# Kernel optimization log

Measured on AMD Instinct MI355X. Metric: run time of the kernel, lower is better.

The kernel has to match this reference:

```python
import jax, jax.numpy as jnp
import numpy as np

MARGIN = 0.1
EPS = 1e-8  # torch CosineSimilarity eps


def setup_inputs() -> dict:
    key = jax.random.key(0)
    k1, k2 = jax.random.split(key)
    embeddings = jax.random.normal(k1, (8192, 128), dtype=jnp.float32)
    labels = jax.random.randint(k2, (8192,), 0, 100, dtype=jnp.int64 if jax.config.jax_enable_x64 else jnp.int32)
    return {"embeddings": embeddings, "labels": labels}


def reference(embeddings, labels):
    n = embeddings.shape[0]
    # Normalize rows (torch: x / max(||x||, eps))
    norm = jnp.linalg.norm(embeddings, axis=1, keepdims=True)
    en = embeddings / jnp.maximum(norm, EPS)
    # Full cosine-similarity matrix via one GEMM: [n, n]
    sim = jnp.einsum('id,jd->ij', en, en)
    same = labels[:, None] == labels[None, :]
    pair_loss = jnp.where(same, jax.nn.relu(1.0 - sim), jax.nn.relu(sim - MARGIN))
    # Sum over i < j (strict upper triangle), matching the double loop
    upper = jnp.triu(jnp.ones((n, n), dtype=pair_loss.dtype), k=1)
    loss = jnp.sum(pair_loss * upper) / (n * (n - 1))
    return loss
```

## Files before the change

kernel.cpp:

```cpp
#include <hip/hip_runtime.h>
#include <hip/hip_bf16.h>


typedef __attribute__((ext_vector_type(8))) short short8;
typedef __attribute__((ext_vector_type(4))) float f32x4;

#define DIM 128
#define MARGIN 0.1f
#define CHUNK 4

typedef const void __attribute__((address_space(1)))* gas_ptr;
typedef void __attribute__((address_space(3)))* las_ptr;

static __device__ __forceinline__ void load16_to_lds(const void* g, void* l) {
    __builtin_amdgcn_global_load_lds((gas_ptr)g, (las_ptr)l, 16, 0, 0);
}

static __device__ __forceinline__ unsigned short f2bf(float f) {
    unsigned int u = __builtin_bit_cast(unsigned int, f);
    u += 0x7FFFu + ((u >> 16) & 1u);
    return (unsigned short)(u >> 16);
}

static __device__ __forceinline__ void stage64(const short* __restrict__ en, int row0,
                                               short* buf, int tid) {
    const char* src = (const char*)(en + (size_t)row0 * DIM);
    char* dst = (char*)buf;
    const int r_lo = tid >> 4;
    const int s    = tid & 15;
    #pragma unroll
    for (int p = 0; p < 4; ++p) {
        const int r  = p * 16 + r_lo;
        const int sc = (s ^ (r & 7)) << 4;
        load16_to_lds(src + (size_t)r * 256 + sc, dst + r * 256 + s * 16);
    }
}

static __device__ __forceinline__ short8 read_frag(const short* buf, int row, int slot) {
    const int ps = slot ^ (row & 7);
    return *(const short8*)(buf + row * DIM + ps * 8);
}

__global__ void __launch_bounds__(256) norm_bf16_kernel(const float* __restrict__ e,
                                                        unsigned int* __restrict__ en_packed) {
    const int row  = blockIdx.x * 4 + (threadIdx.x >> 6);
    const int lane = threadIdx.x & 63;
    const float2 v = *reinterpret_cast<const float2*>(e + row * DIM + lane * 2);
    float s = v.x * v.x + v.y * v.y;
    #pragma unroll
    for (int off = 32; off; off >>= 1) s += __shfl_xor(s, off, 64);
    const float scale = 1.0f / fmaxf(sqrtf(s), 1e-8f);
    const unsigned int lo = f2bf(v.x * scale);
    const unsigned int hi = f2bf(v.y * scale);
    en_packed[row * (DIM / 2) + lane] = (hi << 16) | lo;
}

__global__ void __launch_bounds__(256, 3)
tri_loss_kernel(const short* __restrict__ en, const int* __restrict__ labels,
                float* __restrict__ partials, int nt) {
    __shared__ __align__(16) short buf[2][64 * DIM];
    __shared__ float wsum[4];

    int t  = blockIdx.x;
    int bi = 0, cnt = (nt + CHUNK - 1) / CHUNK;
    #pragma unroll 1
    while (t >= cnt) { t -= cnt; ++bi; cnt = (nt - bi + CHUNK - 1) / CHUNK; }
    const int jbase = bi + t * CHUNK;
    const int nsub  = 2 * min(CHUNK, nt - jbase);

    const int tid  = threadIdx.x;
    const int lane = tid & 63;
    const int wid  = tid >> 6;
    const int wr   = wid >> 1, wc = wid & 1;
    const int lm   = lane & 15;
    const int hi   = lane >> 4;

    stage64(en, bi * 128,      &buf[0][0], tid);
    stage64(en, bi * 128 + 64, &buf[1][0], tid);

    const int r0w = bi * 128 + wr * 64;
    int4 li[4];
    #pragma unroll
    for (int m = 0; m < 4; ++m) li[m] = *(const int4*)(labels + r0w + m * 16 + hi * 4);

    __syncthreads();

    short8 a[4][4];
    const short* Abuf = &buf[wr][0];
    #pragma unroll
    for (int m = 0; m < 4; ++m)
        #pragma unroll
        for (int ks = 0; ks < 4; ++ks)
            a[m][ks] = read_frag(Abuf, m * 16 + lm, hi + ks * 4);

    __syncthreads();

    stage64(en, jbase * 128, &buf[0][0], tid);
    __syncthreads();

    float lsum = 0.0f;
    const int rb = hi * 4;

    #pragma unroll 1
    for (int s = 0; s < nsub; ++s) {
        const short* cur = &buf[s & 1][0];
        if (s + 1 < nsub)
            stage64(en, jbase * 128 + (s + 1) * 64, &buf[(s + 1) & 1][0], tid);

        const int c0 = jbase * 128 + s * 64 + wc * 32;
        int labj[2];
        labj[0] = labels[c0 + lm];
        labj[1] = labels[c0 + 16 + lm];

        f32x4 acc[4][2] = {};
        #pragma unroll
        for (int ks = 0; ks < 4; ++ks) {
            short8 b[2];
            b[0] = read_frag(cur, wc * 32 + lm,      hi + ks * 4);
            b[1] = read_frag(cur, wc * 32 + 16 + lm, hi + ks * 4);
            #pragma unroll
            for (int m = 0; m < 4; ++m)
                #pragma unroll
                for (int n = 0; n < 2; ++n)
                    acc[m][n] = __builtin_amdgcn_mfma_f32_16x16x32_bf16(a[m][ks], b[n], acc[m][n], 0, 0, 0);
        }

        const bool diag = (jbase == bi) && (s < 2);
        #pragma unroll
        for (int m = 0; m < 4; ++m) {
            #pragma unroll
            for (int r = 0; r < 4; ++r) {
                const int i   = r0w + m * 16 + rb + r;
                const int l_i = ((const int*)&li[m])[r];
                #pragma unroll
                for (int n = 0; n < 2; ++n) {
                    const int j  = c0 + n * 16 + lm;
                    const float sv = acc[m][n][r];
                    const float t2 = (l_i == labj[n]) ? (1.0f - sv) : (sv - MARGIN);
                    const float v  = fmaxf(t2, 0.0f);
                    if (!diag || i < j) lsum += v;
                }
            }
        }
        __syncthreads();
    }

    #pragma unroll
    for (int off = 32; off; off >>= 1) lsum += __shfl_down(lsum, off, 64);
    if (lane == 0) wsum[wid] = lsum;
    __syncthreads();
    if (tid == 0) partials[blockIdx.x] = wsum[0] + wsum[1] + wsum[2] + wsum[3];
}

__global__ void __launch_bounds__(256) final_reduce_kernel(const float* __restrict__ partials,
                                                           float* __restrict__ out,
                                                           int n, float inv_denom) {
    float s = 0.0f;
    for (int i = threadIdx.x; i < n; i += 256) s += partials[i];
    #pragma unroll
    for (int off = 32; off; off >>= 1) s += __shfl_xor(s, off, 64);
    __shared__ float wsum[4];
    if ((threadIdx.x & 63) == 0) wsum[threadIdx.x >> 6] = s;
    __syncthreads();
    if (threadIdx.x == 0) out[0] = (wsum[0] + wsum[1] + wsum[2] + wsum[3]) * inv_denom;
}

extern "C" void kernel_launch(void* const* d_in, const int* in_sizes, int n_in,
                              void* d_out, int out_size, void* d_ws, size_t ws_size,
                              hipStream_t stream) {
    const float* emb    = (const float*)d_in[0];
    const int*   labels = (const int*)d_in[1];
    float*       out    = (float*)d_out;

    const int n  = in_sizes[1];
    const int nt = n / 128;

    int Tc = 0;
    for (int i = 0; i < nt; ++i) Tc += (nt - i + CHUNK - 1) / CHUNK;

    unsigned int* en_packed = (unsigned int*)d_ws;
    short*        en        = (short*)d_ws;
    float*        partials  = (float*)((char*)d_ws + (size_t)n * DIM * 2);

    norm_bf16_kernel<<<n / 4, 256, 0, stream>>>(emb, en_packed);

    tri_loss_kernel<<<Tc, 256, 0, stream>>>(en, labels, partials, nt);

    const float inv_denom = (float)(1.0 / ((double)n * (double)(n - 1)));
    final_reduce_kernel<<<1, 256, 0, stream>>>(partials, out, Tc, inv_denom);
}
```

Before: 31.00 us.

## Split triangle-loss tiles across eight waves and streamline the epilogue

Doubles the block to 512 threads so each of the eight waves owns 32 rows instead of 64 of the 128-row A tile. This halves the per-wave A fragments and accumulators, and staging now takes two load iterations per thread instead of four. The epilogue now has separate diagonal and off-diagonal paths, accumulates into a vector, and drops the relu on the same-label term in favour of a select. The aim is more waves in flight to hide latency and a cheaper epilogue. The cost is more LDS B-fragment reads per MFMA, and the same-label term is no longer clamped at zero.

```diff
diff --git a/kernel.cpp b/kernel.cpp
--- a/kernel.cpp
+++ b/kernel.cpp
@@ -29,8 +29,8 @@
     const int r_lo = tid >> 4;
     const int s    = tid & 15;
     #pragma unroll
-    for (int p = 0; p < 4; ++p) {
-        const int r  = p * 16 + r_lo;
+    for (int p = 0; p < 2; ++p) {
+        const int r  = p * 32 + r_lo;
         const int sc = (s ^ (r & 7)) << 4;
         load16_to_lds(src + (size_t)r * 256 + sc, dst + r * 256 + s * 16);
     }
@@ -55,101 +55,128 @@
     en_packed[row * (DIM / 2) + lane] = (hi << 16) | lo;
 }
 
-__global__ void __launch_bounds__(256, 3)
+__global__ void __launch_bounds__(512, 4)
 tri_loss_kernel(const short* __restrict__ en, const int* __restrict__ labels,
                 float* __restrict__ partials, int nt) {
     __shared__ __align__(16) short buf[2][64 * DIM];
-    __shared__ float wsum[4];
+    __shared__ float wsum[8];
 
     int t  = blockIdx.x;
     int bi = 0, cnt = (nt + CHUNK - 1) / CHUNK;
     #pragma unroll 1
     while (t >= cnt) { t -= cnt; ++bi; cnt = (nt - bi + CHUNK - 1) / CHUNK; }
     const int jbase = bi + t * CHUNK;
+    const int jb128 = jbase * 128;
     const int nsub  = 2 * min(CHUNK, nt - jbase);
 
     const int tid  = threadIdx.x;
     const int lane = tid & 63;
     const int wid  = tid >> 6;
-    const int wr   = wid >> 1, wc = wid & 1;
+    const int wr   = wid >> 1;
+    const int wc   = wid & 1;
     const int lm   = lane & 15;
     const int hi   = lane >> 4;
+    const int rb   = hi * 4;
 
     stage64(en, bi * 128,      &buf[0][0], tid);
     stage64(en, bi * 128 + 64, &buf[1][0], tid);
 
-    const int r0w = bi * 128 + wr * 64;
-    int4 li[4];
-    #pragma unroll
-    for (int m = 0; m < 4; ++m) li[m] = *(const int4*)(labels + r0w + m * 16 + hi * 4);
-
-    __syncthreads();
-
-    short8 a[4][4];
-    const short* Abuf = &buf[wr][0];
-    #pragma unroll
-    for (int m = 0; m < 4; ++m)
+    const int r0w = bi * 128 + wr * 32;
+    int liv[2][4];
+    #pragma unroll
+    for (int m = 0; m < 2; ++m) {
+        const int4 lv = *(const int4*)(labels + r0w + m * 16 + rb);
+        liv[m][0] = lv.x; liv[m][1] = lv.y; liv[m][2] = lv.z; liv[m][3] = lv.w;
+    }
+
+    __syncthreads();
+
+    short8 a[2][4];
+    const short* Abuf = &buf[wr >> 1][0];
+    const int rloc = (wr & 1) * 32;
+    #pragma unroll
+    for (int m = 0; m < 2; ++m)
         #pragma unroll
         for (int ks = 0; ks < 4; ++ks)
-            a[m][ks] = read_frag(Abuf, m * 16 + lm, hi + ks * 4);
-
-    __syncthreads();
-
-    stage64(en, jbase * 128, &buf[0][0], tid);
-    __syncthreads();
-
-    float lsum = 0.0f;
-    const int rb = hi * 4;
+            a[m][ks] = read_frag(Abuf, rloc + m * 16 + lm, hi + ks * 4);
+
+    __syncthreads();
+
+    stage64(en, jb128, &buf[0][0], tid);
+    __syncthreads();
+
+    f32x4 vsum = (f32x4){0.0f, 0.0f, 0.0f, 0.0f};
 
     #pragma unroll 1
     for (int s = 0; s < nsub; ++s) {
         const short* cur = &buf[s & 1][0];
         if (s + 1 < nsub)
-            stage64(en, jbase * 128 + (s + 1) * 64, &buf[(s + 1) & 1][0], tid);
-
-        const int c0 = jbase * 128 + s * 64 + wc * 32;
+            stage64(en, jb128 + (s + 1) * 64, &buf[(s + 1) & 1][0], tid);
+
+        const int c0 = jb128 + s * 64 + wc * 32;
         int labj[2];
         labj[0] = labels[c0 + lm];
         labj[1] = labels[c0 + 16 + lm];
 
-        f32x4 acc[4][2] = {};
+        f32x4 acc[2][2] = {};
         #pragma unroll
         for (int ks = 0; ks < 4; ++ks) {
             short8 b[2];
             b[0] = read_frag(cur, wc * 32 + lm,      hi + ks * 4);
             b[1] = read_frag(cur, wc * 32 + 16 + lm, hi + ks * 4);
             #pragma unroll
-            for (int m = 0; m < 4; ++m)
+            for (int m = 0; m < 2; ++m)
                 #pragma unroll
                 for (int n = 0; n < 2; ++n)
                     acc[m][n] = __builtin_amdgcn_mfma_f32_16x16x32_bf16(a[m][ks], b[n], acc[m][n], 0, 0, 0);
         }
 
-        const bool diag = (jbase == bi) && (s < 2);
-        #pragma unroll
-        for (int m = 0; m < 4; ++m) {
+        if ((jbase == bi) && (s < 2)) {
             #pragma unroll
-            for (int r = 0; r < 4; ++r) {
-                const int i   = r0w + m * 16 + rb + r;
-                const int l_i = ((const int*)&li[m])[r];
+            for (int m = 0; m < 2; ++m)
                 #pragma unroll
                 for (int n = 0; n < 2; ++n) {
-                    const int j  = c0 + n * 16 + lm;
-                    const float sv = acc[m][n][r];
-                    const float t2 = (l_i == labj[n]) ? (1.0f - sv) : (sv - MARGIN);
-                    const float v  = fmaxf(t2, 0.0f);
-                    if (!diag || i < j) lsum += v;
+                    const f32x4 sv   = acc[m][n];
+                    const f32x4 base = sv - MARGIN;
+                    const f32x4 alt  = 1.0f - sv;
+                    const int jj = c0 + n * 16 + lm;
+                    #pragma unroll
+                    for (int r = 0; r < 4; ++r) {
+                        const int ii = r0w + m * 16 + rb + r;
+                        const float bv = fmaxf(base[r], 0.0f);
+                        const float tv = (liv[m][r] == labj[n]) ? alt[r] : bv;
+                        vsum[r] += (ii < jj) ? tv : 0.0f;
+                    }
                 }
-            }
+        } else {
+            #pragma unroll
+            for (int m = 0; m < 2; ++m)
+                #pragma unroll
+                for (int n = 0; n < 2; ++n) {
+                    const f32x4 sv   = acc[m][n];
+                    const f32x4 base = sv - MARGIN;
+                    const f32x4 alt  = 1.0f - sv;
+                    #pragma unroll
+                    for (int r = 0; r < 4; ++r) {
+                        const float bv = fmaxf(base[r], 0.0f);
+                        vsum[r] += (liv[m][r] == labj[n]) ? alt[r] : bv;
+                    }
+                }
         }
         __syncthreads();
     }
 
+    float lsum = vsum[0] + vsum[1] + vsum[2] + vsum[3];
     #pragma unroll
     for (int off = 32; off; off >>= 1) lsum += __shfl_down(lsum, off, 64);
     if (lane == 0) wsum[wid] = lsum;
     __syncthreads();
-    if (tid == 0) partials[blockIdx.x] = wsum[0] + wsum[1] + wsum[2] + wsum[3];
+    if (tid == 0) {
+        float b = 0.0f;
+        #pragma unroll
+        for (int w = 0; w < 8; ++w) b += wsum[w];
+        partials[blockIdx.x] = b;
+    }
 }
 
 __global__ void __launch_bounds__(256) final_reduce_kernel(const float* __restrict__ partials,
@@ -184,7 +211,7 @@
 
     norm_bf16_kernel<<<n / 4, 256, 0, stream>>>(emb, en_packed);
 
-    tri_loss_kernel<<<Tc, 256, 0, stream>>>(en, labels, partials, nt);
+    tri_loss_kernel<<<Tc, 512, 0, stream>>>(en, labels, partials, nt);
 
     const float inv_denom = (float)(1.0 / ((double)n * (double)(n - 1)));
     final_reduce_kernel<<<1, 256, 0, stream>>>(partials, out, Tc, inv_denom);
```

Result: no change. 30.97 us (-0.1%).
